# Kernel optimization log

Measured on AMD Instinct MI355X. Metric: run time of the kernel, lower is better.

The kernel has to match this reference:

```python
import jax, jax.numpy as jnp
import numpy as np


def dct_matrix(N):
    # Orthonormal DCT-II matrix: 2D DCT (scipy fftpack dct ortho applied on both axes) = M @ X @ M.T
    n = jnp.arange(N, dtype=jnp.float32)
    M = jnp.cos(jnp.pi * (2.0 * n[None, :] + 1.0) * n[:, None] / (2.0 * N)) * jnp.sqrt(2.0 / N)
    M = M.at[0].multiply(1.0 / jnp.sqrt(2.0))
    return M


def setup_inputs() -> dict:
    key = jax.random.key(0)
    k1, k2, k3, k4, k5 = jax.random.split(key, 5)
    B, T, C, H, W = 8, 32, 3, 224, 224
    images = jax.random.uniform(k1, (B, T, C, H, W), dtype=jnp.float32)
    w1 = jax.random.normal(k2, (256, 128), dtype=jnp.float32) * 0.05
    b1 = jax.random.normal(k3, (256,), dtype=jnp.float32) * 0.05
    w2 = jax.random.normal(k4, (768, 256), dtype=jnp.float32) * 0.05
    b2 = jax.random.normal(k5, (768,), dtype=jnp.float32) * 0.05
    return {"images": images, "w1": w1, "b1": b1, "w2": w2, "b2": b2}


def reference(images, w1, b1, w2, b2):
    B, T, C, H, W = images.shape
    # (img*255).astype(np.uint8): truncation toward zero (inputs in [0,1) so floor)
    u8 = jnp.floor(jnp.clip(images * 255.0, 0.0, 255.0))
    # cv2.COLOR_RGB2GRAY: Y = 0.299R + 0.587G + 0.114B, rounded to uint8
    gray = jnp.round(0.299 * u8[:, :, 0] + 0.587 * u8[:, :, 1] + 0.114 * u8[:, :, 2])  # [B,T,H,W]
    # Full-frame 2D orthonormal DCT-II via matmul (H == W assumed)
    M = dct_matrix(H)
    dct = jnp.einsum('ih,bthw,jw->btij', M, gray, M)  # [B,T,H,W]
    # Block feature extraction: for each 32-strided block origin, keep dct[i:i+8, j:j+8].flatten()[:16]
    nbi, nbj = H // 32, W // 32
    rows = (jnp.arange(nbi) * 32)[:, None] + jnp.arange(2)   # [nbi,2]
    cols = (jnp.arange(nbj) * 32)[:, None] + jnp.arange(8)   # [nbj,8]
    sub = jnp.take(dct, rows.reshape(-1), axis=2)            # [B,T,nbi*2,W]
    sub = jnp.take(sub, cols.reshape(-1), axis=3)            # [B,T,nbi*2,nbj*8]
    sub = sub.reshape(B, T, nbi, 2, nbj, 8).transpose(0, 1, 2, 4, 3, 5).reshape(B, T, -1)
    feats = sub[:, :, :128].astype(jnp.float32)              # [B,T,128]
    # fc: Linear(128,256) -> ReLU -> Dropout(eval: identity) -> Linear(256, embed_dim)
    h = jax.nn.relu(jnp.einsum('btf,of->bto', feats, w1) + b1)
    return jnp.einsum('bth,oh->bto', h, w2) + b2
```

## Files before the change

### kernel.cpp

```cpp
#include <hip/hip_runtime.h>
#include <math.h>

#define HW 224
#define NCOL 56

__device__ __forceinline__ float dctM(int r, int k) {
    int m = ((2 * k + 1) * r) % (4 * HW);
    float ang = (float)m * (3.14159265358979323846f / (2.0f * HW));
    float v = cosf(ang);
    v *= (r == 0) ? 0.06681531047810609f : 0.09449111825230679f;
    return v;
}

__device__ __forceinline__ float gray_px(float r, float g, float b) {
    float ru = floorf(r * 255.f);
    float gu = floorf(g * 255.f);
    float bu = floorf(b * 255.f);
    return rintf(fmaf(0.299f, ru, fmaf(0.587f, gu, 0.114f * bu)));
}

__global__ __launch_bounds__(512) void k1_feats(const float* __restrict__ img,
                                                float* __restrict__ feats) {
    __shared__ float msel[4 * HW];
    __shared__ float tmp[4 * HW];
    __shared__ float buf[HW * NCOL];

    const int tid = threadIdx.x;
    const int frame = blockIdx.x;

    for (int idx = tid; idx < 4 * HW; idx += 512) {
        int i = idx / HW, h = idx % HW;
        int r = (i < 2) ? i : (30 + i);
        msel[idx] = dctM(r, h);
    }
    __syncthreads();

    const int cg = tid & 63;
    const int strip = tid >> 6;
    if (cg < 56) {
        const float* p = img + (size_t)frame * (3 * HW * HW) + (strip * 28) * HW + cg * 4;
        float4 a0 = {0, 0, 0, 0}, a1 = {0, 0, 0, 0}, a2 = {0, 0, 0, 0}, a3 = {0, 0, 0, 0};
        #pragma unroll 4
        for (int h = 0; h < 28; ++h) {
            const float4 r4 = *(const float4*)(p + h * HW);
            const float4 g4 = *(const float4*)(p + HW * HW + h * HW);
            const float4 b4 = *(const float4*)(p + 2 * HW * HW + h * HW);
            float gx = gray_px(r4.x, g4.x, b4.x);
            float gy = gray_px(r4.y, g4.y, b4.y);
            float gz = gray_px(r4.z, g4.z, b4.z);
            float gw = gray_px(r4.w, g4.w, b4.w);
            int hh = strip * 28 + h;
            float m0 = msel[0 * HW + hh];
            float m1 = msel[1 * HW + hh];
            float m2 = msel[2 * HW + hh];
            float m3 = msel[3 * HW + hh];
            a0.x += m0 * gx; a0.y += m0 * gy; a0.z += m0 * gz; a0.w += m0 * gw;
            a1.x += m1 * gx; a1.y += m1 * gy; a1.z += m1 * gz; a1.w += m1 * gw;
            a2.x += m2 * gx; a2.y += m2 * gy; a2.z += m2 * gz; a2.w += m2 * gw;
            a3.x += m3 * gx; a3.y += m3 * gy; a3.z += m3 * gz; a3.w += m3 * gw;
        }
        float* tp = buf + strip * (4 * HW) + cg * 4;
        *(float4*)(tp + 0 * HW) = a0;
        *(float4*)(tp + 1 * HW) = a1;
        *(float4*)(tp + 2 * HW) = a2;
        *(float4*)(tp + 3 * HW) = a3;
    }
    __syncthreads();

    for (int idx = tid; idx < 4 * HW; idx += 512) {
        float s = 0.f;
        #pragma unroll
        for (int st = 0; st < 8; ++st) s += buf[st * (4 * HW) + idx];
        tmp[idx] = s;
    }
    __syncthreads();

    for (int idx = tid; idx < HW * NCOL; idx += 512) {
        int w = idx / NCOL, jj = idx % NCOL;
        int j = ((jj >> 3) << 5) + (jj & 7);
        buf[idx] = dctM(j, w);
    }
    __syncthreads();

    if (tid < 4 * NCOL) {
        int i = tid / NCOL, jj = tid % NCOL;
        float s = 0.f;
        #pragma unroll 8
        for (int w2 = 0; w2 < HW; ++w2)
            s += tmp[i * HW + w2] * buf[w2 * NCOL + jj];
        int f = -1;
        if (i < 2) {
            f = (jj >> 3) * 16 + i * 8 + (jj & 7);
        } else if (jj < 8) {
            f = 112 + (i - 2) * 8 + jj;
        }
        if (f >= 0) feats[frame * 128 + f] = s;
    }
}

__global__ __launch_bounds__(256) void k2_fc1(const float* __restrict__ feats,
                                              const float* __restrict__ w1,
                                              const float* __restrict__ b1,
                                              float* __restrict__ hbuf) {
    __shared__ float sA[16 * 129];
    __shared__ float sW[16 * 129];
    const int tid = threadIdx.x;
    const int fg = blockIdx.x, og = blockIdx.y;
    for (int idx = tid; idx < 16 * 128; idx += 256) {
        int r = idx >> 7, c = idx & 127;
        sA[r * 129 + c] = feats[(fg * 16 + r) * 128 + c];
        sW[r * 129 + c] = w1[(og * 16 + r) * 128 + c];
    }
    __syncthreads();
    const int fr = tid >> 4, o = tid & 15;
    float s = 0.f;
    #pragma unroll 8
    for (int f = 0; f < 128; ++f)
        s += sA[fr * 129 + f] * sW[o * 129 + f];
    s += b1[og * 16 + o];
    hbuf[(fg * 16 + fr) * 256 + og * 16 + o] = fmaxf(s, 0.f);
}

__global__ __launch_bounds__(256) void k3_fc2(const float* __restrict__ hbuf,
                                              const float* __restrict__ w2,
                                              const float* __restrict__ b2,
                                              float* __restrict__ out) {
    __shared__ float sH[16 * 257];
    __shared__ float sW[16 * 257];
    const int tid = threadIdx.x;
    const int fg = blockIdx.x, eg = blockIdx.y;
    for (int idx = tid; idx < 16 * 256; idx += 256) {
        int r = idx >> 8, c = idx & 255;
        sH[r * 257 + c] = hbuf[(fg * 16 + r) * 256 + c];
        sW[r * 257 + c] = w2[(eg * 16 + r) * 256 + c];
    }
    __syncthreads();
    const int fr = tid >> 4, e = tid & 15;
    float s = 0.f;
    #pragma unroll 8
    for (int k = 0; k < 256; ++k)
        s += sH[fr * 257 + k] * sW[e * 257 + k];
    s += b2[eg * 16 + e];
    out[(fg * 16 + fr) * 768 + eg * 16 + e] = s;
}

extern "C" void kernel_launch(void* const* d_in, const int* in_sizes, int n_in,
                              void* d_out, int out_size, void* d_ws, size_t ws_size,
                              hipStream_t stream) {
    const float* img = (const float*)d_in[0];
    const float* w1  = (const float*)d_in[1];
    const float* b1  = (const float*)d_in[2];
    const float* w2  = (const float*)d_in[3];
    const float* b2  = (const float*)d_in[4];
    float* out = (float*)d_out;

    float* feats = (float*)d_ws;
    float* hbuf  = feats + 256 * 128;

    k1_feats<<<256, 512, 0, stream>>>(img, feats);
    k2_fc1<<<dim3(16, 16), 256, 0, stream>>>(feats, w1, b1, hbuf);
    k3_fc2<<<dim3(16, 48), 256, 0, stream>>>(hbuf, w2, b2, out);
}
```

Baseline: 52.00 us.

## Split row projection across 2048 blocks and fuse column DCT with fc1

The image-reading row-DCT stage now runs over 2048 blocks (frame × 8 row strips) instead of 256, to fill more CUs for the bandwidth-bound read of about 154 MB. Partial sums go to global memory and are reduced in a second kernel, which also does the column projection and fc1 per frame. fc2 is retiled so each block reuses weight chunks across 8 frames. This adds a global round trip for the partials and keeps the same three launches.

```diff
diff --git a/kernel.cpp b/kernel.cpp
--- a/kernel.cpp
+++ b/kernel.cpp
@@ -19,29 +19,30 @@
     return rintf(fmaf(0.299f, ru, fmaf(0.587f, gu, 0.114f * bu)));
 }
 
-__global__ __launch_bounds__(512) void k1_feats(const float* __restrict__ img,
-                                                float* __restrict__ feats) {
-    __shared__ float msel[4 * HW];
-    __shared__ float tmp[4 * HW];
-    __shared__ float buf[HW * NCOL];
+__global__ __launch_bounds__(256, 4) void kA_rowproj(const float* __restrict__ img,
+                                                     float* __restrict__ gpart) {
+    __shared__ float msel[4 * 28];
+    __shared__ float part[4 * 4 * HW];
 
     const int tid = threadIdx.x;
-    const int frame = blockIdx.x;
+    const int bid = blockIdx.x;
+    const int frame = bid >> 3, strip = bid & 7;
 
-    for (int idx = tid; idx < 4 * HW; idx += 512) {
-        int i = idx / HW, h = idx % HW;
+    if (tid < 112) {
+        int i = tid / 28, h = tid % 28;
         int r = (i < 2) ? i : (30 + i);
-        msel[idx] = dctM(r, h);
+        msel[i * 28 + h] = dctM(r, strip * 28 + h);
     }
     __syncthreads();
 
     const int cg = tid & 63;
-    const int strip = tid >> 6;
+    const int sub = tid >> 6;
     if (cg < 56) {
-        const float* p = img + (size_t)frame * (3 * HW * HW) + (strip * 28) * HW + cg * 4;
+        const float* p = img + (size_t)frame * (3 * HW * HW)
+                       + (strip * 28 + sub * 7) * HW + cg * 4;
         float4 a0 = {0, 0, 0, 0}, a1 = {0, 0, 0, 0}, a2 = {0, 0, 0, 0}, a3 = {0, 0, 0, 0};
-        #pragma unroll 4
-        for (int h = 0; h < 28; ++h) {
+        #pragma unroll
+        for (int h = 0; h < 7; ++h) {
             const float4 r4 = *(const float4*)(p + h * HW);
             const float4 g4 = *(const float4*)(p + HW * HW + h * HW);
             const float4 b4 = *(const float4*)(p + 2 * HW * HW + h * HW);
@@ -49,17 +50,17 @@
             float gy = gray_px(r4.y, g4.y, b4.y);
             float gz = gray_px(r4.z, g4.z, b4.z);
             float gw = gray_px(r4.w, g4.w, b4.w);
-            int hh = strip * 28 + h;
-            float m0 = msel[0 * HW + hh];
-            float m1 = msel[1 * HW + hh];
-            float m2 = msel[2 * HW + hh];
-            float m3 = msel[3 * HW + hh];
+            int hh = sub * 7 + h;
+            float m0 = msel[0 * 28 + hh];
+            float m1 = msel[1 * 28 + hh];
+            float m2 = msel[2 * 28 + hh];
+            float m3 = msel[3 * 28 + hh];
             a0.x += m0 * gx; a0.y += m0 * gy; a0.z += m0 * gz; a0.w += m0 * gw;
             a1.x += m1 * gx; a1.y += m1 * gy; a1.z += m1 * gz; a1.w += m1 * gw;
             a2.x += m2 * gx; a2.y += m2 * gy; a2.z += m2 * gz; a2.w += m2 * gw;
             a3.x += m3 * gx; a3.y += m3 * gy; a3.z += m3 * gz; a3.w += m3 * gw;
         }
-        float* tp = buf + strip * (4 * HW) + cg * 4;
+        float* tp = part + sub * (4 * HW) + cg * 4;
         *(float4*)(tp + 0 * HW) = a0;
         *(float4*)(tp + 1 * HW) = a1;
         *(float4*)(tp + 2 * HW) = a2;
@@ -67,18 +68,34 @@
     }
     __syncthreads();
 
-    for (int idx = tid; idx < 4 * HW; idx += 512) {
+    for (int idx = tid; idx < 4 * HW; idx += 256) {
+        float s = part[idx] + part[896 + idx] + part[2 * 896 + idx] + part[3 * 896 + idx];
+        gpart[bid * 896 + idx] = s;
+    }
+}
+
+__global__ __launch_bounds__(256) void kB_proj_fc1(const float* __restrict__ gpart,
+                                                   const float* __restrict__ w1,
+                                                   const float* __restrict__ b1,
+                                                   float* __restrict__ hbuf) {
+    __shared__ float tmp[4 * HW];
+    __shared__ float mcol[HW * NCOL];
+    __shared__ float feats[128];
+
+    const int tid = threadIdx.x;
+    const int frame = blockIdx.x;
+
+    for (int idx = tid; idx < 4 * HW; idx += 256) {
+        const float* g = gpart + (size_t)frame * 8 * 896 + idx;
         float s = 0.f;
         #pragma unroll
-        for (int st = 0; st < 8; ++st) s += buf[st * (4 * HW) + idx];
+        for (int st = 0; st < 8; ++st) s += g[st * 896];
         tmp[idx] = s;
     }
-    __syncthreads();
-
-    for (int idx = tid; idx < HW * NCOL; idx += 512) {
+    for (int idx = tid; idx < HW * NCOL; idx += 256) {
         int w = idx / NCOL, jj = idx % NCOL;
         int j = ((jj >> 3) << 5) + (jj & 7);
-        buf[idx] = dctM(j, w);
+        mcol[idx] = dctM(j, w);
     }
     __syncthreads();
 
@@ -86,62 +103,68 @@
         int i = tid / NCOL, jj = tid % NCOL;
         float s = 0.f;
         #pragma unroll 8
-        for (int w2 = 0; w2 < HW; ++w2)
-            s += tmp[i * HW + w2] * buf[w2 * NCOL + jj];
+        for (int w = 0; w < HW; ++w)
+            s += tmp[i * HW + w] * mcol[w * NCOL + jj];
         int f = -1;
-        if (i < 2) {
-            f = (jj >> 3) * 16 + i * 8 + (jj & 7);
-        } else if (jj < 8) {
-            f = 112 + (i - 2) * 8 + jj;
-        }
-        if (f >= 0) feats[frame * 128 + f] = s;
+        if (i < 2)        f = (jj >> 3) * 16 + i * 8 + (jj & 7);
+        else if (jj < 8)  f = 112 + (i - 2) * 8 + jj;
+        if (f >= 0) feats[f] = s;
     }
+    __syncthreads();
+
+    float acc = b1[tid];
+    const float4* wrow = (const float4*)(w1 + tid * 128);
+    #pragma unroll 8
+    for (int f4 = 0; f4 < 32; ++f4) {
+        float4 w4 = wrow[f4];
+        float4 x4 = *(const float4*)(feats + 4 * f4);
+        acc += w4.x * x4.x + w4.y * x4.y + w4.z * x4.z + w4.w * x4.w;
+    }
+    hbuf[frame * 256 + tid] = fmaxf(acc, 0.f);
 }
 
-__global__ __launch_bounds__(256) void k2_fc1(const float* __restrict__ feats,
-                                              const float* __restrict__ w1,
-                                              const float* __restrict__ b1,
-                                              float* __restrict__ hbuf) {
-    __shared__ float sA[16 * 129];
-    __shared__ float sW[16 * 129];
-    const int tid = threadIdx.x;
-    const int fg = blockIdx.x, og = blockIdx.y;
-    for (int idx = tid; idx < 16 * 128; idx += 256) {
-        int r = idx >> 7, c = idx & 127;
-        sA[r * 129 + c] = feats[(fg * 16 + r) * 128 + c];
-        sW[r * 129 + c] = w1[(og * 16 + r) * 128 + c];
-    }
-    __syncthreads();
-    const int fr = tid >> 4, o = tid & 15;
-    float s = 0.f;
-    #pragma unroll 8
-    for (int f = 0; f < 128; ++f)
-        s += sA[fr * 129 + f] * sW[o * 129 + f];
-    s += b1[og * 16 + o];
-    hbuf[(fg * 16 + fr) * 256 + og * 16 + o] = fmaxf(s, 0.f);
-}
-
-__global__ __launch_bounds__(256) void k3_fc2(const float* __restrict__ hbuf,
+#define KC_FR 8
+__global__ __launch_bounds__(256) void kC_fc2(const float* __restrict__ hbuf,
                                               const float* __restrict__ w2,
                                               const float* __restrict__ b2,
                                               float* __restrict__ out) {
-    __shared__ float sH[16 * 257];
-    __shared__ float sW[16 * 257];
+    __shared__ float sH[KC_FR * 256];
+    __shared__ float sW[256 * 36];
+
     const int tid = threadIdx.x;
-    const int fg = blockIdx.x, eg = blockIdx.y;
-    for (int idx = tid; idx < 16 * 256; idx += 256) {
-        int r = idx >> 8, c = idx & 255;
-        sH[r * 257 + c] = hbuf[(fg * 16 + r) * 256 + c];
-        sW[r * 257 + c] = w2[(eg * 16 + r) * 256 + c];
+    const int fg = blockIdx.x;
+    const int og = blockIdx.y;
+
+    for (int idx = tid; idx < KC_FR * 256; idx += 256)
+        sH[idx] = hbuf[(fg * KC_FR + (idx >> 8)) * 256 + (idx & 255)];
+
+    float acc[KC_FR];
+    #pragma unroll
+    for (int f = 0; f < KC_FR; ++f) acc[f] = 0.f;
+
+    for (int kc = 0; kc < 256; kc += 32) {
+        __syncthreads();
+        for (int idx = tid; idx < 256 * 32; idx += 256) {
+            int o = idx >> 5, k = idx & 31;
+            sW[o * 36 + k] = w2[(og * 256 + o) * 256 + kc + k];
+        }
+        __syncthreads();
+        const float4* wr = (const float4*)(sW + tid * 36);
+        #pragma unroll
+        for (int k4 = 0; k4 < 8; ++k4) {
+            float4 w4 = wr[k4];
+            #pragma unroll
+            for (int f = 0; f < KC_FR; ++f) {
+                float4 h4 = *(const float4*)(sH + f * 256 + kc + 4 * k4);
+                acc[f] += w4.x * h4.x + w4.y * h4.y + w4.z * h4.z + w4.w * h4.w;
+            }
+        }
     }
-    __syncthreads();
-    const int fr = tid >> 4, e = tid & 15;
-    float s = 0.f;
-    #pragma unroll 8
-    for (int k = 0; k < 256; ++k)
-        s += sH[fr * 257 + k] * sW[e * 257 + k];
-    s += b2[eg * 16 + e];
-    out[(fg * 16 + fr) * 768 + eg * 16 + e] = s;
+
+    float bb = b2[og * 256 + tid];
+    #pragma unroll
+    for (int f = 0; f < KC_FR; ++f)
+        out[(fg * KC_FR + f) * 768 + og * 256 + tid] = acc[f] + bb;
 }
 
 extern "C" void kernel_launch(void* const* d_in, const int* in_sizes, int n_in,
@@ -154,10 +177,10 @@
     const float* b2  = (const float*)d_in[4];
     float* out = (float*)d_out;
 
-    float* feats = (float*)d_ws;
-    float* hbuf  = feats + 256 * 128;
+    float* gpart = (float*)d_ws;
+    float* hbuf  = gpart + 2048 * 896;
 
-    k1_feats<<<256, 512, 0, stream>>>(img, feats);
-    k2_fc1<<<dim3(16, 16), 256, 0, stream>>>(feats, w1, b1, hbuf);
-    k3_fc2<<<dim3(16, 48), 256, 0, stream>>>(hbuf, w2, b2, out);
+    kA_rowproj<<<2048, 256, 0, stream>>>(img, gpart);
+    kB_proj_fc1<<<256, 256, 0, stream>>>(gpart, w1, b1, hbuf);
+    kC_fc2<<<dim3(32, 3), 256, 0, stream>>>(hbuf, w2, b2, out);
 }
```

New measurement: 71.69 us. 37.9% more time.

## Fuse DCT feature extraction and both FC layers into one kernel

Applied to the files above, without the earlier changes.

Merges the feature kernel and the two linear-layer kernels into a single per-frame kernel. Features and hidden activations stay in shared memory instead of going through a global workspace, and the two extra launches are removed. In exchange, every block now reads the full w1 and w2 matrices, with one weight row per thread, so the loads are strided and uncoalesced.

```diff
diff --git a/kernel.cpp b/kernel.cpp
--- a/kernel.cpp
+++ b/kernel.cpp
@@ -19,19 +19,25 @@
     return rintf(fmaf(0.299f, ru, fmaf(0.587f, gu, 0.114f * bu)));
 }
 
-__global__ __launch_bounds__(512) void k1_feats(const float* __restrict__ img,
-                                                float* __restrict__ feats) {
+__global__ __launch_bounds__(512) void k_fused(const float* __restrict__ img,
+                                               const float* __restrict__ w1,
+                                               const float* __restrict__ b1,
+                                               const float* __restrict__ w2,
+                                               const float* __restrict__ b2,
+                                               float* __restrict__ out) {
     __shared__ float msel[4 * HW];
     __shared__ float tmp[4 * HW];
     __shared__ float buf[HW * NCOL];
+    __shared__ float feats[128];
+    __shared__ float h[256];
 
     const int tid = threadIdx.x;
     const int frame = blockIdx.x;
 
     for (int idx = tid; idx < 4 * HW; idx += 512) {
-        int i = idx / HW, h = idx % HW;
+        int i = idx / HW, hh = idx % HW;
         int r = (i < 2) ? i : (30 + i);
-        msel[idx] = dctM(r, h);
+        msel[idx] = dctM(r, hh);
     }
     __syncthreads();
 
@@ -41,19 +47,19 @@
         const float* p = img + (size_t)frame * (3 * HW * HW) + (strip * 28) * HW + cg * 4;
         float4 a0 = {0, 0, 0, 0}, a1 = {0, 0, 0, 0}, a2 = {0, 0, 0, 0}, a3 = {0, 0, 0, 0};
         #pragma unroll 4
-        for (int h = 0; h < 28; ++h) {
-            const float4 r4 = *(const float4*)(p + h * HW);
-            const float4 g4 = *(const float4*)(p + HW * HW + h * HW);
-            const float4 b4 = *(const float4*)(p + 2 * HW * HW + h * HW);
+        for (int hh = 0; hh < 28; ++hh) {
+            const float4 r4 = *(const float4*)(p + hh * HW);
+            const float4 g4 = *(const float4*)(p + HW * HW + hh * HW);
+            const float4 b4 = *(const float4*)(p + 2 * HW * HW + hh * HW);
             float gx = gray_px(r4.x, g4.x, b4.x);
             float gy = gray_px(r4.y, g4.y, b4.y);
             float gz = gray_px(r4.z, g4.z, b4.z);
             float gw = gray_px(r4.w, g4.w, b4.w);
-            int hh = strip * 28 + h;
-            float m0 = msel[0 * HW + hh];
-            float m1 = msel[1 * HW + hh];
-            float m2 = msel[2 * HW + hh];
-            float m3 = msel[3 * HW + hh];
+            int hi = strip * 28 + hh;
+            float m0 = msel[0 * HW + hi];
+            float m1 = msel[1 * HW + hi];
+            float m2 = msel[2 * HW + hi];
+            float m3 = msel[3 * HW + hi];
             a0.x += m0 * gx; a0.y += m0 * gy; a0.z += m0 * gz; a0.w += m0 * gw;
             a1.x += m1 * gx; a1.y += m1 * gy; a1.z += m1 * gz; a1.w += m1 * gw;
             a2.x += m2 * gx; a2.y += m2 * gy; a2.z += m2 * gz; a2.w += m2 * gw;
@@ -86,62 +92,51 @@
         int i = tid / NCOL, jj = tid % NCOL;
         float s = 0.f;
         #pragma unroll 8
-        for (int w2 = 0; w2 < HW; ++w2)
-            s += tmp[i * HW + w2] * buf[w2 * NCOL + jj];
+        for (int w2i = 0; w2i < HW; ++w2i)
+            s += tmp[i * HW + w2i] * buf[w2i * NCOL + jj];
         int f = -1;
-        if (i < 2) {
-            f = (jj >> 3) * 16 + i * 8 + (jj & 7);
-        } else if (jj < 8) {
-            f = 112 + (i - 2) * 8 + jj;
-        }
-        if (f >= 0) feats[frame * 128 + f] = s;
-    }
-}
-
-__global__ __launch_bounds__(256) void k2_fc1(const float* __restrict__ feats,
-                                              const float* __restrict__ w1,
-                                              const float* __restrict__ b1,
-                                              float* __restrict__ hbuf) {
-    __shared__ float sA[16 * 129];
-    __shared__ float sW[16 * 129];
-    const int tid = threadIdx.x;
-    const int fg = blockIdx.x, og = blockIdx.y;
-    for (int idx = tid; idx < 16 * 128; idx += 256) {
-        int r = idx >> 7, c = idx & 127;
-        sA[r * 129 + c] = feats[(fg * 16 + r) * 128 + c];
-        sW[r * 129 + c] = w1[(og * 16 + r) * 128 + c];
+        if (i < 2)        f = (jj >> 3) * 16 + i * 8 + (jj & 7);
+        else if (jj < 8)  f = 112 + (i - 2) * 8 + jj;
+        if (f >= 0) feats[f] = s;
     }
     __syncthreads();
-    const int fr = tid >> 4, o = tid & 15;
-    float s = 0.f;
-    #pragma unroll 8
-    for (int f = 0; f < 128; ++f)
-        s += sA[fr * 129 + f] * sW[o * 129 + f];
-    s += b1[og * 16 + o];
-    hbuf[(fg * 16 + fr) * 256 + og * 16 + o] = fmaxf(s, 0.f);
-}
 
-__global__ __launch_bounds__(256) void k3_fc2(const float* __restrict__ hbuf,
-                                              const float* __restrict__ w2,
-                                              const float* __restrict__ b2,
-                                              float* __restrict__ out) {
-    __shared__ float sH[16 * 257];
-    __shared__ float sW[16 * 257];
-    const int tid = threadIdx.x;
-    const int fg = blockIdx.x, eg = blockIdx.y;
-    for (int idx = tid; idx < 16 * 256; idx += 256) {
-        int r = idx >> 8, c = idx & 255;
-        sH[r * 257 + c] = hbuf[(fg * 16 + r) * 256 + c];
-        sW[r * 257 + c] = w2[(eg * 16 + r) * 256 + c];
+    if (tid < 256) {
+        float acc = b1[tid];
+        const float4* wrow = (const float4*)(w1 + tid * 128);
+        #pragma unroll 8
+        for (int f4 = 0; f4 < 32; ++f4) {
+            float4 w4 = wrow[f4];
+            float4 x4 = *(const float4*)(feats + 4 * f4);
+            acc += w4.x * x4.x + w4.y * x4.y + w4.z * x4.z + w4.w * x4.w;
+        }
+        h[tid] = fmaxf(acc, 0.f);
     }
     __syncthreads();
-    const int fr = tid >> 4, e = tid & 15;
-    float s = 0.f;
-    #pragma unroll 8
-    for (int k = 0; k < 256; ++k)
-        s += sH[fr * 257 + k] * sW[e * 257 + k];
-    s += b2[eg * 16 + e];
-    out[(fg * 16 + fr) * 768 + eg * 16 + e] = s;
+
+    {
+        float acc = b2[tid];
+        const float4* wrow = (const float4*)(w2 + tid * 256);
+        #pragma unroll 8
+        for (int k4 = 0; k4 < 64; ++k4) {
+            float4 w4 = wrow[k4];
+            float4 h4 = *(const float4*)(h + 4 * k4);
+            acc += w4.x * h4.x + w4.y * h4.y + w4.z * h4.z + w4.w * h4.w;
+        }
+        out[(size_t)frame * 768 + tid] = acc;
+    }
+    if (tid < 256) {
+        int e = 512 + tid;
+        float acc = b2[e];
+        const float4* wrow = (const float4*)(w2 + e * 256);
+        #pragma unroll 8
+        for (int k4 = 0; k4 < 64; ++k4) {
+            float4 w4 = wrow[k4];
+            float4 h4 = *(const float4*)(h + 4 * k4);
+            acc += w4.x * h4.x + w4.y * h4.y + w4.z * h4.z + w4.w * h4.w;
+        }
+        out[(size_t)frame * 768 + e] = acc;
+    }
 }
 
 extern "C" void kernel_launch(void* const* d_in, const int* in_sizes, int n_in,
@@ -154,10 +149,5 @@
     const float* b2  = (const float*)d_in[4];
     float* out = (float*)d_out;
 
-    float* feats = (float*)d_ws;
-    float* hbuf  = feats + 256 * 128;
-
-    k1_feats<<<256, 512, 0, stream>>>(img, feats);
-    k2_fc1<<<dim3(16, 16), 256, 0, stream>>>(feats, w1, b1, hbuf);
-    k3_fc2<<<dim3(16, 48), 256, 0, stream>>>(hbuf, w2, b2, out);
+    k_fused<<<256, 512, 0, stream>>>(img, w1, b1, w2, b2, out);
 }
```

Result: slower. 59.17 us (+13.8%).
